# Performance work log

Hardware: AMD Instinct MI355X
Metric: run time of the kernel (lower is better)

## Reference

```python
import jax, jax.numpy as jnp
import numpy as np


def setup_inputs() -> dict:
    key = jax.random.key(0)
    k1, k2, k3 = jax.random.split(key, 3)
    b, c, h, w = 4, 64, 64, 64
    content = jax.random.normal(k1, (b, c, h, w), dtype=jnp.float32)
    content_s = jax.random.normal(k2, (b, c, h, w), dtype=jnp.float32)
    style = jax.random.normal(k3, (b, c, h, w), dtype=jnp.float32)
    return {"content": content, "content_s": content_s, "style": style}


def reference(content, content_s, style):
    b, c, h, w = content.shape
    hw = h * w
    Fc = content.reshape(b, c, hw)      # [b, c, HW]
    Fs = content_s.reshape(b, c, hw)    # [b, c, HW]
    Fst = style.reshape(b, c, hw)       # [b, c, HW]
    # S[b, q, k] = sum_c Fc[b, c, q] * Fs[b, c, k]  (Fc transposed as in torch)
    S = jnp.einsum('bcq,bck->bqk', Fc, Fs)
    S = jax.nn.softmax(S, axis=-1)
    # O = style @ S^T : O[b, c, q] = sum_k Fst[b, c, k] * S[b, q, k]
    O = jnp.einsum('bck,bqk->bcq', Fst, S).reshape(b, c, h, w)
    return jnp.concatenate((content, O), axis=1)
```

## Files before the change

### kernel.cpp

```cpp
#include <hip/hip_runtime.h>
#include <math.h>


#define Bb 4
#define Cc 64
#define HWs 4096
#define RLOG2E 1.44269504088896340736f
#define DEFER_THR 6.0f

typedef _Float16 half8 __attribute__((ext_vector_type(8)));
typedef _Float16 half4 __attribute__((ext_vector_type(4)));
typedef float floatx4 __attribute__((ext_vector_type(4)));
typedef unsigned uint2v __attribute__((ext_vector_type(2)));

__global__ __launch_bounds__(256) void prep_k(const float* __restrict__ content,
                                              const float* __restrict__ Fs,
                                              const float* __restrict__ Fst,
                                              float* __restrict__ out,
                                              _Float16* __restrict__ Kt,
                                              _Float16* __restrict__ Vt) {
    const int bid = blockIdx.x;
    const int t = threadIdx.x;
    if (bid < 1024) {
        int i4 = bid * 256 + t;
        const float4* c4 = (const float4*)content;
        const float4* v4 = (const float4*)Fst;
        float4* o4 = (float4*)out;
        int b = i4 >> 16, rem = i4 & 65535;
        o4[(size_t)b * 131072 + rem] = c4[i4];
        float4 v = v4[i4];
        half4 h;
        h[0] = (_Float16)v.x; h[1] = (_Float16)v.y;
        h[2] = (_Float16)v.z; h[3] = (_Float16)v.w;
        *(half4*)(Vt + (size_t)i4 * 4) = h;
    } else {
        __shared__ _Float16 T[16][72];
        int e = bid - 1024;
        int b = e >> 8;
        int hw0 = (e & 255) * 16;
        const float* sb = Fs + (size_t)b * Cc * HWs;
        {
            int c = t >> 2, x4 = (t & 3) * 4;
            float4 v = *(const float4*)(sb + (size_t)c * HWs + hw0 + x4);
            T[x4 + 0][c] = (_Float16)v.x;
            T[x4 + 1][c] = (_Float16)v.y;
            T[x4 + 2][c] = (_Float16)v.z;
            T[x4 + 3][c] = (_Float16)v.w;
        }
        __syncthreads();
        if (t < 128) {
            int row = t >> 3, g = t & 7;
            _Float16* db = Kt + (size_t)b * HWs * Cc;
            *(half8*)(db + (size_t)(hw0 + row) * Cc + g * 8) = *(half8*)&T[row][g * 8];
        }
    }
}

template <int NS>
__global__ __launch_bounds__(256, 4) void attn_k(const float* __restrict__ Fc,
                                                 const _Float16* __restrict__ Kt,
                                                 const _Float16* __restrict__ Vt,
                                                 _Float16* __restrict__ Opart,
                                                 float2* __restrict__ ml) {
    constexpr int TPS = 64 / NS;
    const int tid  = threadIdx.x;
    const int w    = tid >> 6;
    const int lane = tid & 63;
    const int quad = lane >> 4;
    const int l15  = lane & 15;
    const int qg = blockIdx.x & 31;
    const int b  = (blockIdx.x >> 5) & 3;
    const int s  = blockIdx.x >> 7;
    const int k0base = s * TPS * 64;
    const int qA = qg * 128 + w * 32 + l15;
    const int qB = qA + 16;

    __shared__ _Float16 Kl[2][64 * 64];
    __shared__ _Float16 Vl[2][64 * 64];

    const float*    Fcb = Fc + (size_t)b * Cc * HWs;
    const _Float16* Kb  = Kt + (size_t)b * HWs * Cc;
    const _Float16* Vb  = Vt + (size_t)b * Cc * HWs;

    const int lrow = lane >> 3;
    const int lj   = lane & 7;
    const int lsw8 = (lj ^ lrow) * 8;
    const int r0   = w * 16;

    auto stage = [&](int kt, int p) {
        const int kk0 = k0base + kt * 64;
        #pragma unroll
        for (int c = 0; c < 2; ++c) {
            const int r = r0 + c * 8 + lrow;
            __builtin_amdgcn_global_load_lds(
                (const __attribute__((address_space(1))) void*)(Kb + (size_t)(kk0 + r) * 64 + lsw8),
                (__attribute__((address_space(3))) void*)&Kl[p][(r0 + c * 8) * 64],
                16, 0, 0);
            __builtin_amdgcn_global_load_lds(
                (const __attribute__((address_space(1))) void*)(Vb + (size_t)r * HWs + kk0 + lsw8),
                (__attribute__((address_space(3))) void*)&Vl[p][(r0 + c * 8) * 64],
                16, 0, 0);
        }
    };

    half8 qf[2][2];
    #pragma unroll
    for (int j = 0; j < 8; ++j) {
        qf[0][0][j] = (_Float16)(Fcb[(size_t)(quad * 8 + j) * HWs + qA] * RLOG2E);
        qf[0][1][j] = (_Float16)(Fcb[(size_t)(32 + quad * 8 + j) * HWs + qA] * RLOG2E);
        qf[1][0][j] = (_Float16)(Fcb[(size_t)(quad * 8 + j) * HWs + qB] * RLOG2E);
        qf[1][1][j] = (_Float16)(Fcb[(size_t)(32 + quad * 8 + j) * HWs + qB] * RLOG2E);
    }

    floatx4 acc[2][4];
    #pragma unroll
    for (int g = 0; g < 2; ++g)
        #pragma unroll
        for (int m = 0; m < 4; ++m) acc[g][m] = (floatx4)(0.0f);
    float m_run[2] = {-INFINITY, -INFINITY};
    float lsum[2] = {0.0f, 0.0f};

    stage(0, 0);
    __syncthreads();

    const int swl = (l15 & 7);
    for (int kt = 0; kt < TPS; ++kt) {
        const int p = kt & 1;
        if (kt + 1 < TPS) stage(kt + 1, p ^ 1);

        floatx4 sv[2][4];
        __builtin_amdgcn_s_setprio(1);
        #pragma unroll
        for (int m = 0; m < 4; ++m) {
            const half8 ka0 = *(const half8*)&Kl[p][(m * 16 + l15) * 64 + ((quad ^ swl) * 8)];
            const half8 ka1 = *(const half8*)&Kl[p][(m * 16 + l15) * 64 + (((4 + quad) ^ swl) * 8)];
            sv[0][m] = __builtin_amdgcn_mfma_f32_16x16x32_f16(ka0, qf[0][0], (floatx4)(0.0f), 0, 0, 0);
            sv[0][m] = __builtin_amdgcn_mfma_f32_16x16x32_f16(ka1, qf[0][1], sv[0][m], 0, 0, 0);
            sv[1][m] = __builtin_amdgcn_mfma_f32_16x16x32_f16(ka0, qf[1][0], (floatx4)(0.0f), 0, 0, 0);
            sv[1][m] = __builtin_amdgcn_mfma_f32_16x16x32_f16(ka1, qf[1][1], sv[1][m], 0, 0, 0);
        }
        __builtin_amdgcn_s_setprio(0);

        half8 pb[2][2];
        #pragma unroll
        for (int g = 0; g < 2; ++g) {
            float mx = sv[g][0][0];
            #pragma unroll
            for (int m = 0; m < 4; ++m)
                #pragma unroll
                for (int r = 0; r < 4; ++r) mx = fmaxf(mx, sv[g][m][r]);
            {
                unsigned mu = __float_as_uint(mx);
                uint2v t32 = __builtin_amdgcn_permlane32_swap(mu, mu, false, false);
                mx = fmaxf(__uint_as_float(t32[0]), __uint_as_float(t32[1]));
                mu = __float_as_uint(mx);
                uint2v t16 = __builtin_amdgcn_permlane16_swap(mu, mu, false, false);
                mx = fmaxf(__uint_as_float(t16[0]), __uint_as_float(t16[1]));
            }
            if (!__all(mx - m_run[g] <= DEFER_THR)) {
                float m_new = fmaxf(m_run[g], mx);
                float alpha = exp2f(m_run[g] - m_new);
                m_run[g] = m_new;
                #pragma unroll
                for (int m = 0; m < 4; ++m) acc[g][m] *= alpha;
                lsum[g] *= alpha;
            }
            const float mb = m_run[g];
            unsigned Ap[4], Bp[4];
            #pragma unroll
            for (int m = 0; m < 4; ++m) {
                float e0 = exp2f(sv[g][m][0] - mb);
                float e1 = exp2f(sv[g][m][1] - mb);
                float e2 = exp2f(sv[g][m][2] - mb);
                float e3 = exp2f(sv[g][m][3] - mb);
                lsum[g] += (e0 + e1) + (e2 + e3);
                Ap[m] = __builtin_bit_cast(unsigned, __builtin_amdgcn_cvt_pkrtz(e0, e1));
                Bp[m] = __builtin_bit_cast(unsigned, __builtin_amdgcn_cvt_pkrtz(e2, e3));
            }
            unsigned pw[2][4];
            { uint2v a = __builtin_amdgcn_permlane32_swap(Ap[0], Ap[1], false, false);
              uint2v u = __builtin_amdgcn_permlane16_swap(a[0], a[1], false, false);
              pw[0][0] = u[0]; pw[0][2] = u[1]; }
            { uint2v a = __builtin_amdgcn_permlane32_swap(Bp[0], Bp[1], false, false);
              uint2v u = __builtin_amdgcn_permlane16_swap(a[0], a[1], false, false);
              pw[0][1] = u[0]; pw[0][3] = u[1]; }
            { uint2v a = __builtin_amdgcn_permlane32_swap(Ap[2], Ap[3], false, false);
              uint2v u = __builtin_amdgcn_permlane16_swap(a[0], a[1], false, false);
              pw[1][0] = u[0]; pw[1][2] = u[1]; }
            { uint2v a = __builtin_amdgcn_permlane32_swap(Bp[2], Bp[3], false, false);
              uint2v u = __builtin_amdgcn_permlane16_swap(a[0], a[1], false, false);
              pw[1][1] = u[0]; pw[1][3] = u[1]; }
            #pragma unroll
            for (int ks = 0; ks < 2; ++ks) {
                union { unsigned u4[4]; half8 h; } z;
                z.u4[0] = pw[ks][0]; z.u4[1] = pw[ks][1];
                z.u4[2] = pw[ks][2]; z.u4[3] = pw[ks][3];
                pb[g][ks] = z.h;
            }
        }

        __builtin_amdgcn_s_setprio(1);
        #pragma unroll
        for (int m = 0; m < 4; ++m) {
            const half8 va0 = *(const half8*)&Vl[p][(m * 16 + l15) * 64 + ((quad ^ swl) * 8)];
            const half8 va1 = *(const half8*)&Vl[p][(m * 16 + l15) * 64 + (((4 + quad) ^ swl) * 8)];
            acc[0][m] = __builtin_amdgcn_mfma_f32_16x16x32_f16(va0, pb[0][0], acc[0][m], 0, 0, 0);
            acc[0][m] = __builtin_amdgcn_mfma_f32_16x16x32_f16(va1, pb[0][1], acc[0][m], 0, 0, 0);
            acc[1][m] = __builtin_amdgcn_mfma_f32_16x16x32_f16(va0, pb[1][0], acc[1][m], 0, 0, 0);
            acc[1][m] = __builtin_amdgcn_mfma_f32_16x16x32_f16(va1, pb[1][1], acc[1][m], 0, 0, 0);
        }
        __builtin_amdgcn_s_setprio(0);

        __syncthreads();
    }

    _Float16* op = Opart + ((size_t)(s * Bb + b) * Cc) * HWs;
    #pragma unroll
    for (int g = 0; g < 2; ++g) {
        lsum[g] += __shfl_xor(lsum[g], 16);
        lsum[g] += __shfl_xor(lsum[g], 32);
        int q = (g == 0) ? qA : qB;
        #pragma unroll
        for (int m = 0; m < 4; ++m)
            #pragma unroll
            for (int r = 0; r < 4; ++r) {
                int c = m * 16 + quad * 4 + r;
                op[(size_t)c * HWs + q] = (_Float16)acc[g][m][r];
            }
        if (quad == 0)
            ml[((size_t)b * HWs + q) * NS + s] = make_float2(m_run[g], lsum[g]);
    }
}

template <int NS>
__global__ __launch_bounds__(256) void combine_k(const _Float16* __restrict__ Opart,
                                                 const float2* __restrict__ ml,
                                                 float* __restrict__ out) {
    int idx = blockIdx.x * 256 + threadIdx.x;
    int q = idx & 4095;
    int c = (idx >> 12) & 63;
    int b = idx >> 18;
    const float2* mlp = ml + ((size_t)b * HWs + q) * NS;
    float2 mls[NS];
    #pragma unroll
    for (int s = 0; s < NS; ++s) mls[s] = mlp[s];
    float M = -INFINITY;
    #pragma unroll
    for (int s = 0; s < NS; ++s) M = fmaxf(M, mls[s].x);
    float l = 0.0f, o = 0.0f;
    #pragma unroll
    for (int s = 0; s < NS; ++s) {
        float wgt = exp2f(mls[s].x - M);
        l += wgt * mls[s].y;
        o += wgt * (float)Opart[(((size_t)s * Bb + b) * Cc + c) * HWs + q];
    }
    out[((size_t)b * 2 * Cc + Cc + c) * HWs + q] = o / l;
}

extern "C" void kernel_launch(void* const* d_in, const int* in_sizes, int n_in,
                              void* d_out, int out_size, void* d_ws, size_t ws_size,
                              hipStream_t stream) {
    const float* content   = (const float*)d_in[0];
    const float* content_s = (const float*)d_in[1];
    const float* style     = (const float*)d_in[2];
    float* out = (float*)d_out;

    _Float16* Kt = (_Float16*)d_ws;
    _Float16* Vt = Kt + (size_t)Bb * HWs * Cc;
    _Float16* Opart = Vt + (size_t)Bb * Cc * HWs;

    const size_t base = (size_t)2 * Bb * HWs * Cc * sizeof(_Float16);
    const size_t need8 = base + (size_t)8 * Bb * Cc * HWs * sizeof(_Float16)
                              + (size_t)Bb * HWs * 8 * sizeof(float2);
    const int ns = (ws_size >= need8) ? 8 : 4;
    float2* ml = (float2*)(Opart + (size_t)ns * Bb * Cc * HWs);

    prep_k<<<dim3(2048), dim3(256), 0, stream>>>(content, content_s, style, out, Kt, Vt);
    if (ns == 8) {
        attn_k<8><<<dim3(8 * Bb * 32), dim3(256), 0, stream>>>(content, Kt, Vt, Opart, ml);
        combine_k<8><<<dim3(4096), dim3(256), 0, stream>>>(Opart, ml, out);
    } else {
        attn_k<4><<<dim3(4 * Bb * 32), dim3(256), 0, stream>>>(content, Kt, Vt, Opart, ml);
        combine_k<4><<<dim3(4096), dim3(256), 0, stream>>>(Opart, ml, out);
    }
}
```

Measured before the change: 111.2 us.

## Load K/V fragments directly from global into registers, drop LDS staging

```diff
diff --git a/kernel.cpp b/kernel.cpp
--- a/kernel.cpp
+++ b/kernel.cpp
@@ -57,7 +57,7 @@
 }
 
 template <int NS>
-__global__ __launch_bounds__(256, 4) void attn_k(const float* __restrict__ Fc,
+__global__ __launch_bounds__(256, 2) void attn_k(const float* __restrict__ Fc,
                                                  const _Float16* __restrict__ Kt,
                                                  const _Float16* __restrict__ Vt,
                                                  _Float16* __restrict__ Opart,
@@ -75,32 +75,25 @@
     const int qA = qg * 128 + w * 32 + l15;
     const int qB = qA + 16;
 
-    __shared__ _Float16 Kl[2][64 * 64];
-    __shared__ _Float16 Vl[2][64 * 64];
-
     const float*    Fcb = Fc + (size_t)b * Cc * HWs;
-    const _Float16* Kb  = Kt + (size_t)b * HWs * Cc;
-    const _Float16* Vb  = Vt + (size_t)b * Cc * HWs;
-
-    const int lrow = lane >> 3;
-    const int lj   = lane & 7;
-    const int lsw8 = (lj ^ lrow) * 8;
-    const int r0   = w * 16;
-
-    auto stage = [&](int kt, int p) {
-        const int kk0 = k0base + kt * 64;
-        #pragma unroll
-        for (int c = 0; c < 2; ++c) {
-            const int r = r0 + c * 8 + lrow;
-            __builtin_amdgcn_global_load_lds(
-                (const __attribute__((address_space(1))) void*)(Kb + (size_t)(kk0 + r) * 64 + lsw8),
-                (__attribute__((address_space(3))) void*)&Kl[p][(r0 + c * 8) * 64],
-                16, 0, 0);
-            __builtin_amdgcn_global_load_lds(
-                (const __attribute__((address_space(1))) void*)(Vb + (size_t)r * HWs + kk0 + lsw8),
-                (__attribute__((address_space(3))) void*)&Vl[p][(r0 + c * 8) * 64],
-                16, 0, 0);
-        }
+    const _Float16* Kfl = Kt + (size_t)b * HWs * Cc + (size_t)l15 * 64 + quad * 8;
+    const _Float16* Vfl = Vt + (size_t)b * Cc * HWs + (size_t)l15 * HWs + quad * 8;
+
+    auto loadK = [&](int kt, half8 (&ka)[4][2]) {
+        const _Float16* p = Kfl + (size_t)(k0base + kt * 64) * 64;
+        #pragma unroll
+        for (int m = 0; m < 4; ++m)
+            #pragma unroll
+            for (int cs = 0; cs < 2; ++cs)
+                ka[m][cs] = *(const half8*)(p + m * 1024 + cs * 32);
+    };
+    auto loadV = [&](int kt, half8 (&va)[4][2]) {
+        const _Float16* p = Vfl + (k0base + kt * 64);
+        #pragma unroll
+        for (int m = 0; m < 4; ++m)
+            #pragma unroll
+            for (int ks = 0; ks < 2; ++ks)
+                va[m][ks] = *(const half8*)(p + (size_t)m * 16 * HWs + ks * 32);
     };
 
     half8 qf[2][2];
@@ -120,45 +113,36 @@
     float m_run[2] = {-INFINITY, -INFINITY};
     float lsum[2] = {0.0f, 0.0f};
 
-    stage(0, 0);
-    __syncthreads();
-
-    const int swl = (l15 & 7);
-    for (int kt = 0; kt < TPS; ++kt) {
-        const int p = kt & 1;
-        if (kt + 1 < TPS) stage(kt + 1, p ^ 1);
-
-        floatx4 sv[2][4];
+    floatx4 sv[2][4];
+    auto s_mfma = [&](half8 (&ka)[4][2]) {
         __builtin_amdgcn_s_setprio(1);
         #pragma unroll
         for (int m = 0; m < 4; ++m) {
-            const half8 ka0 = *(const half8*)&Kl[p][(m * 16 + l15) * 64 + ((quad ^ swl) * 8)];
-            const half8 ka1 = *(const half8*)&Kl[p][(m * 16 + l15) * 64 + (((4 + quad) ^ swl) * 8)];
-            sv[0][m] = __builtin_amdgcn_mfma_f32_16x16x32_f16(ka0, qf[0][0], (floatx4)(0.0f), 0, 0, 0);
-            sv[0][m] = __builtin_amdgcn_mfma_f32_16x16x32_f16(ka1, qf[0][1], sv[0][m], 0, 0, 0);
-            sv[1][m] = __builtin_amdgcn_mfma_f32_16x16x32_f16(ka0, qf[1][0], (floatx4)(0.0f), 0, 0, 0);
-            sv[1][m] = __builtin_amdgcn_mfma_f32_16x16x32_f16(ka1, qf[1][1], sv[1][m], 0, 0, 0);
+            sv[0][m] = __builtin_amdgcn_mfma_f32_16x16x32_f16(ka[m][0], qf[0][0], (floatx4)(0.0f), 0, 0, 0);
+            sv[0][m] = __builtin_amdgcn_mfma_f32_16x16x32_f16(ka[m][1], qf[0][1], sv[0][m], 0, 0, 0);
+            sv[1][m] = __builtin_amdgcn_mfma_f32_16x16x32_f16(ka[m][0], qf[1][0], (floatx4)(0.0f), 0, 0, 0);
+            sv[1][m] = __builtin_amdgcn_mfma_f32_16x16x32_f16(ka[m][1], qf[1][1], sv[1][m], 0, 0, 0);
         }
         __builtin_amdgcn_s_setprio(0);
-
+    };
+
+    auto sm_pv = [&](half8 (&va)[4][2]) {
         half8 pb[2][2];
         #pragma unroll
         for (int g = 0; g < 2; ++g) {
-            float mx = sv[g][0][0];
-            #pragma unroll
-            for (int m = 0; m < 4; ++m)
-                #pragma unroll
-                for (int r = 0; r < 4; ++r) mx = fmaxf(mx, sv[g][m][r]);
-            {
+            float mm0 = fmaxf(fmaxf(sv[g][0][0], sv[g][0][1]), fmaxf(sv[g][0][2], sv[g][0][3]));
+            float mm1 = fmaxf(fmaxf(sv[g][1][0], sv[g][1][1]), fmaxf(sv[g][1][2], sv[g][1][3]));
+            float mm2 = fmaxf(fmaxf(sv[g][2][0], sv[g][2][1]), fmaxf(sv[g][2][2], sv[g][2][3]));
+            float mm3 = fmaxf(fmaxf(sv[g][3][0], sv[g][3][1]), fmaxf(sv[g][3][2], sv[g][3][3]));
+            float mx = fmaxf(fmaxf(mm0, mm1), fmaxf(mm2, mm3));
+            if (!__all(mx - m_run[g] <= DEFER_THR)) {
                 unsigned mu = __float_as_uint(mx);
                 uint2v t32 = __builtin_amdgcn_permlane32_swap(mu, mu, false, false);
-                mx = fmaxf(__uint_as_float(t32[0]), __uint_as_float(t32[1]));
-                mu = __float_as_uint(mx);
+                float wmx = fmaxf(__uint_as_float(t32[0]), __uint_as_float(t32[1]));
+                mu = __float_as_uint(wmx);
                 uint2v t16 = __builtin_amdgcn_permlane16_swap(mu, mu, false, false);
-                mx = fmaxf(__uint_as_float(t16[0]), __uint_as_float(t16[1]));
-            }
-            if (!__all(mx - m_run[g] <= DEFER_THR)) {
-                float m_new = fmaxf(m_run[g], mx);
+                wmx = fmaxf(__uint_as_float(t16[0]), __uint_as_float(t16[1]));
+                float m_new = fmaxf(m_run[g], wmx);
                 float alpha = exp2f(m_run[g] - m_new);
                 m_run[g] = m_new;
                 #pragma unroll
@@ -198,20 +182,33 @@
                 pb[g][ks] = z.h;
             }
         }
-
         __builtin_amdgcn_s_setprio(1);
         #pragma unroll
         for (int m = 0; m < 4; ++m) {
-            const half8 va0 = *(const half8*)&Vl[p][(m * 16 + l15) * 64 + ((quad ^ swl) * 8)];
-            const half8 va1 = *(const half8*)&Vl[p][(m * 16 + l15) * 64 + (((4 + quad) ^ swl) * 8)];
-            acc[0][m] = __builtin_amdgcn_mfma_f32_16x16x32_f16(va0, pb[0][0], acc[0][m], 0, 0, 0);
-            acc[0][m] = __builtin_amdgcn_mfma_f32_16x16x32_f16(va1, pb[0][1], acc[0][m], 0, 0, 0);
-            acc[1][m] = __builtin_amdgcn_mfma_f32_16x16x32_f16(va0, pb[1][0], acc[1][m], 0, 0, 0);
-            acc[1][m] = __builtin_amdgcn_mfma_f32_16x16x32_f16(va1, pb[1][1], acc[1][m], 0, 0, 0);
+            acc[0][m] = __builtin_amdgcn_mfma_f32_16x16x32_f16(va[m][0], pb[0][0], acc[0][m], 0, 0, 0);
+            acc[0][m] = __builtin_amdgcn_mfma_f32_16x16x32_f16(va[m][1], pb[0][1], acc[0][m], 0, 0, 0);
+            acc[1][m] = __builtin_amdgcn_mfma_f32_16x16x32_f16(va[m][0], pb[1][0], acc[1][m], 0, 0, 0);
+            acc[1][m] = __builtin_amdgcn_mfma_f32_16x16x32_f16(va[m][1], pb[1][1], acc[1][m], 0, 0, 0);
         }
         __builtin_amdgcn_s_setprio(0);
-
-        __syncthreads();
+    };
+
+    half8 kaA[4][2], kaB[4][2], va[4][2];
+    loadK(0, kaA);
+
+    #pragma unroll 1
+    for (int kt = 0; kt < TPS; kt += 2) {
+        s_mfma(kaA);
+        if (kt + 1 < TPS) loadK(kt + 1, kaB);
+        loadV(kt, va);
+        sm_pv(va);
+
+        if (kt + 1 < TPS) {
+            s_mfma(kaB);
+            if (kt + 2 < TPS) loadK(kt + 2, kaA);
+            loadV(kt + 1, va);
+            sm_pv(va);
+        }
     }
 
     _Float16* op = Opart + ((size_t)(s * Bb + b) * Cc) * HWs;
@@ -268,19 +265,9 @@
     _Float16* Kt = (_Float16*)d_ws;
     _Float16* Vt = Kt + (size_t)Bb * HWs * Cc;
     _Float16* Opart = Vt + (size_t)Bb * Cc * HWs;
-
-    const size_t base = (size_t)2 * Bb * HWs * Cc * sizeof(_Float16);
-    const size_t need8 = base + (size_t)8 * Bb * Cc * HWs * sizeof(_Float16)
-                              + (size_t)Bb * HWs * 8 * sizeof(float2);
-    const int ns = (ws_size >= need8) ? 8 : 4;
-    float2* ml = (float2*)(Opart + (size_t)ns * Bb * Cc * HWs);
+    float2*   ml = (float2*)(Opart + (size_t)4 * Bb * Cc * HWs);
 
     prep_k<<<dim3(2048), dim3(256), 0, stream>>>(content, content_s, style, out, Kt, Vt);
-    if (ns == 8) {
-        attn_k<8><<<dim3(8 * Bb * 32), dim3(256), 0, stream>>>(content, Kt, Vt, Opart, ml);
-        combine_k<8><<<dim3(4096), dim3(256), 0, stream>>>(Opart, ml, out);
-    } else {
-        attn_k<4><<<dim3(4 * Bb * 32), dim3(256), 0, stream>>>(content, Kt, Vt, Opart, ml);
-        combine_k<4><<<dim3(4096), dim3(256), 0, stream>>>(Opart, ml, out);
-    }
-}
+    attn_k<4><<<dim3(4 * Bb * 32), dim3(256), 0, stream>>>(content, Kt, Vt, Opart, ml);
+    combine_k<4><<<dim3(4096), dim3(256), 0, stream>>>(Opart, ml, out);
+}
```

Measured after the change: 134.0 us. +20.6%, slower.
